# Performance work log

Measured on AMD Instinct MI355X. Metric: run time of the kernel, lower is better.

Reference implementation:

```python
import jax, jax.numpy as jnp
import numpy as np
from jax import lax

HID = 768          # hidden_dim / embedding_dim
IN = 64            # input_dim = max_seq_length // num_heads
SEQ = 512          # max_seq_length
GROUPS = IN        # conv groups
BLUR_K = 5
BLUR_SIGMA = 1.0


def _gauss1d(k, sigma):
    half = (k - 1) * 0.5
    x = np.linspace(-half, half, k)
    pdf = np.exp(-0.5 * (x / sigma) ** 2)
    return pdf / pdf.sum()


def setup_inputs() -> dict:
    key = jax.random.key(0)
    ks = jax.random.split(key, 8)
    s = 0.02
    return {
        "inputs": jax.random.normal(ks[0], (16, SEQ, HID), jnp.float32),
        # Conv1d(768, 768, k=3, groups=64): weight [out_ch, in_ch/groups, k]
        "conv_w": jax.random.normal(ks[1], (HID, HID // GROUPS, 3), jnp.float32) * s,
        "conv_b": jnp.zeros((HID,), jnp.float32),
        "ln_g": jnp.ones((IN,), jnp.float32),
        "ln_b": jnp.zeros((IN,), jnp.float32),
        # function_info: Linear(64, 64), torch weight convention [out, in]
        "fi_w": jax.random.normal(ks[2], (IN, IN), jnp.float32) * s,
        "fi_b": jnp.zeros((IN,), jnp.float32),
        # block_info: Linear(64, 1)
        "bi_w": jax.random.normal(ks[3], (1, IN), jnp.float32) * s,
        "bi_b": jnp.zeros((1,), jnp.float32),
    }


def _forward(inputs, conv_w, conv_b, ln_g, ln_b, fi_w, fi_b, bi_w, bi_b):
    x = inputs.reshape(-1, HID, IN)  # [Bn, 768, 64] (raw row-major view, as torch .view)
    q = k = v = m = x

    # q: grouped Conv1d + residual, GELU, LayerNorm over last dim (64)
    qc = lax.conv_general_dilated(
        q, conv_w, window_strides=(1,), padding=[(1, 1)],
        feature_group_count=GROUPS, dimension_numbers=("NCH", "OIH", "NCH"))
    qc = qc + conv_b[None, :, None]
    q = jax.nn.gelu(qc + q, approximate=False)
    mu = jnp.mean(q, axis=-1, keepdims=True)
    var = jnp.mean(jnp.square(q - mu), axis=-1, keepdims=True)
    q = (q - mu) * lax.rsqrt(var + 1e-5) * ln_g + ln_b

    # v: Linear(64,64) + GELU
    v = jax.nn.gelu(v @ fi_w.T + fi_b, approximate=False)

    # k: dropout (eval -> identity), softmax over dim=-2 (channel axis), GELU
    k = jax.nn.gelu(jax.nn.softmax(k, axis=-2), approximate=False)

    # m: GaussianBlur(5, sigma fixed 1.0) over (H=768, W=64) with reflect pad, then Linear(64,1)
    g = _gauss1d(BLUR_K, BLUR_SIGMA)
    kern = jnp.asarray(np.outer(g, g), m.dtype)[None, None]  # [1,1,5,5]
    p = BLUR_K // 2
    mp = jnp.pad(m[:, None], ((0, 0), (0, 0), (p, p), (p, p)), mode="reflect")
    m = lax.conv_general_dilated(
        mp, kern, (1, 1), "VALID", dimension_numbers=("NCHW", "OIHW", "NCHW"))[:, 0]
    m = m @ bi_w.T + bi_b                        # [Bn, 768, 1]
    mask = jnp.broadcast_to(m, (m.shape[0], HID, HID))  # expand to [Bn,768,768]

    # SDPA: scale = 1/sqrt(E) with E = q.shape[-1] = 64; additive float mask
    scores = jnp.einsum("bce,bde->bcd", q, k) * (1.0 / np.sqrt(IN)) + mask
    attn = jax.nn.softmax(scores, axis=-1)
    out = jnp.einsum("bcd,bde->bce", attn, v)    # [Bn, 768, 64]
    return out.reshape(-1, SEQ, HID)


def reference(inputs, conv_w, conv_b, ln_g, ln_b, fi_w, fi_b, bi_w, bi_b):
    return _forward(inputs, conv_w, conv_b, ln_g, ln_b, fi_w, fi_b, bi_w, bi_b)
```

## Files before the change

kernel.cpp:

```cpp
#include <hip/hip_runtime.h>
#include <hip/hip_bf16.h>
#include <math.h>

#define NB 128
#define NC 768
#define NE 64
#define IPG 12

#define QSCALE 0.18033688011112042f

typedef __hip_bfloat16 bf16;
typedef __bf16 bf16v8 __attribute__((ext_vector_type(8)));
typedef __bf16 bf16v4 __attribute__((ext_vector_type(4)));
typedef __bf16 bf16v2 __attribute__((ext_vector_type(2)));
typedef float f32x4 __attribute__((ext_vector_type(4)));
typedef float f32x16 __attribute__((ext_vector_type(16)));
typedef unsigned int u32;
typedef u32 u32x4 __attribute__((ext_vector_type(4)));

__device__ __forceinline__ float gelu_exact(float x) {
    float ax = fabsf(x);
    float t = __builtin_amdgcn_rcpf(fmaf(0.2316419f, ax, 1.0f));
    float poly = t * fmaf(t, fmaf(t, fmaf(t, fmaf(t, 1.330274429f,
                  -1.821255978f), 1.781477937f), -0.356563782f), 0.319381530f);
    float pdf = 0.3989422804f * __expf(-0.5f * ax * ax);
    float c = fmaf(-pdf, poly, 1.0f);
    float cdf = (x >= 0.f) ? c : 1.0f - c;
    return x * cdf;
}

#define MFMA16(a, b, c) __builtin_amdgcn_mfma_f32_16x16x32_bf16(a, b, c, 0, 0, 0)
#define MFMA32(a, b, c) __builtin_amdgcn_mfma_f32_32x32x16_bf16(a, b, c, 0, 0, 0)

__device__ __forceinline__ void gload_lds16(const void* g, void* l) {
    __builtin_amdgcn_global_load_lds(
        (const __attribute__((address_space(1))) void*)g,
        (__attribute__((address_space(3))) void*)l, 16, 0, 0);
}

__device__ __forceinline__ u32 pkbf(float a, float b) {
    bf16v2 t; t[0] = (__bf16)a; t[1] = (__bf16)b;
    return __builtin_bit_cast(u32, t);
}

__global__ __launch_bounds__(256) void k_conv(
    const float* __restrict__ x, const float* __restrict__ cw,
    const float* __restrict__ cb, const float* __restrict__ lg,
    const float* __restrict__ lb, bf16* __restrict__ qo,
    float* __restrict__ sp)
{
    int b = blockIdx.x >> 4;
    int chunk = blockIdx.x & 15;
    int w = threadIdx.x >> 6;
    int g = __builtin_amdgcn_readfirstlane(chunk * 4 + w);
    int h = threadIdx.x & 63;
    const float* xb = x + ((size_t)b * NC + g * IPG) * NE;

    float xi[IPG], xm[IPG], xp[IPG];
    #pragma unroll
    for (int i = 0; i < IPG; ++i) {
        xi[i] = xb[i * NE + h];
        float up = __shfl_up(xi[i], 1);
        float dn = __shfl_down(xi[i], 1);
        xm[i] = h ? up : 0.f;
        xp[i] = (h < 63) ? dn : 0.f;
    }

    float es = 0.f;
    #pragma unroll
    for (int i = 0; i < IPG; ++i) es += __expf(xi[i]);
    __shared__ float red[4][64];
    red[w][h] = es;
    __syncthreads();
    if (w == 0) {
        float s = red[0][h] + red[1][h] + red[2][h] + red[3][h];
        sp[(size_t)(b * 16 + chunk) * 64 + h] = s;
    }

    float gam = lg[h], bet = lb[h];
    const float* wg = cw + (size_t)g * IPG * 36;

    for (int o = 0; o < IPG; ++o) {
        const float* wo = wg + o * 36;
        float acc = cb[g * IPG + o];
        #pragma unroll
        for (int i = 0; i < IPG; ++i)
            acc = fmaf(xm[i], wo[i*3], fmaf(xi[i], wo[i*3+1], fmaf(xp[i], wo[i*3+2], acc)));
        float gl = gelu_exact(acc + xi[o]);
        float s1 = gl, s2 = gl * gl;
        #pragma unroll
        for (int off = 32; off; off >>= 1) {
            s1 += __shfl_xor(s1, off);
            s2 += __shfl_xor(s2, off);
        }
        float mu  = s1 * (1.f / 64.f);
        float var = s2 * (1.f / 64.f) - mu * mu;
        float qn = (gl - mu) * rsqrtf(var + 1e-5f) * gam + bet;
        qo[((size_t)b * NC + g * IPG + o) * NE + h] = __float2bfloat16(qn * QSCALE);
    }
}

__global__ __launch_bounds__(256) void k_vk(
    const float* __restrict__ x, const float* __restrict__ fw,
    const float* __restrict__ fb, const float* __restrict__ sp,
    bf16* __restrict__ ko, bf16* __restrict__ vTo)
{
    int chunk = blockIdx.x, b = blockIdx.y;
    int tid = threadIdx.x, w = tid >> 6, l = tid & 63;
    int lr = l & 15, lc = (l >> 4) * 8;
    int rowb = chunk * 64 + w * 16;
    const float* xb = x + (size_t)b * NC * NE;

    __shared__ float sts[64];
    if (tid < 64) {
        float s = 0.f;
        #pragma unroll
        for (int p = 0; p < 16; ++p) s += sp[(size_t)(b * 16 + p) * 64 + tid];
        sts[tid] = 1.f / s;
    }

    bf16v8 bfr[4][2];
    float fbias[4];
    #pragma unroll
    for (int nt = 0; nt < 4; ++nt) {
        #pragma unroll
        for (int kt = 0; kt < 2; ++kt) {
            const float* p = fw + (nt*16 + lr) * 64 + kt*32 + lc;
            bf16v8 t;
            #pragma unroll
            for (int j = 0; j < 8; ++j) t[j] = (__bf16)p[j];
            bfr[nt][kt] = t;
        }
        fbias[nt] = fb[nt*16 + lr];
    }
    __syncthreads();

    float isA[8], isB[8];
    #pragma unroll
    for (int j = 0; j < 8; ++j) { isA[j] = sts[lc + j]; isB[j] = sts[32 + lc + j]; }

    const float* pa = xb + (size_t)(rowb + lr) * NE;
    float xa[8], xc[8];
    #pragma unroll
    for (int j = 0; j < 8; ++j) xa[j] = pa[lc + j];
    #pragma unroll
    for (int j = 0; j < 8; ++j) xc[j] = pa[32 + lc + j];

    bf16v8 a0, a1;
    #pragma unroll
    for (int j = 0; j < 8; ++j) a0[j] = (__bf16)xa[j];
    #pragma unroll
    for (int j = 0; j < 8; ++j) a1[j] = (__bf16)xc[j];

    bf16v8 kv0, kv1;
    #pragma unroll
    for (int j = 0; j < 8; ++j) kv0[j] = (__bf16)gelu_exact(__expf(xa[j]) * isA[j]);
    #pragma unroll
    for (int j = 0; j < 8; ++j) kv1[j] = (__bf16)gelu_exact(__expf(xc[j]) * isB[j]);
    bf16* kp = ko + ((size_t)b * NC + rowb + lr) * NE + lc;
    *(bf16v8*)kp = kv0;
    *(bf16v8*)(kp + 32) = kv1;

    #pragma unroll
    for (int nt = 0; nt < 4; ++nt) {
        f32x4 acc = {fbias[nt], fbias[nt], fbias[nt], fbias[nt]};
        acc = MFMA16(a0, bfr[nt][0], acc);
        acc = MFMA16(a1, bfr[nt][1], acc);
        bf16v4 pk;
        #pragma unroll
        for (int r = 0; r < 4; ++r) pk[r] = (__bf16)gelu_exact(acc[r]);
        int c = rowb + (l >> 4) * 4;
        *(bf16v4*)&vTo[((size_t)b * NE + nt*16 + lr) * NC + c] = pk;
    }
}

__global__ __launch_bounds__(256, 3) void k_attn(const bf16* __restrict__ qb,
                                                 const bf16* __restrict__ kb,
                                                 const bf16* __restrict__ vT,
                                                 float* __restrict__ out) {
    __shared__ __align__(16) __bf16 ldsK[2][4096];
    __shared__ __align__(16) __bf16 ldsV[2][4096];

    int bid = blockIdx.x;
    int swz = (bid & 7) * 96 + (bid >> 3);
    int b = swz / 6, qt = swz - b * 6;
    int w = threadIdx.x >> 6, l = threadIdx.x & 63;
    int q0 = qt * 128 + w * 32;
    int l31 = l & 31, b5 = l >> 5;

    int krow_ = w * 8 + (l >> 3);
    int kc16_ = (l & 7) ^ (l >> 3);
    const char* kgbase = (const char*)(kb + (size_t)b * NC * NE)
                       + krow_ * 128 + kc16_ * 16;
    int ve_   = w * 16 + (l >> 2);
    int vc16_ = (l & 3) ^ ((l >> 3) & 3);
    const char* vgbase = (const char*)(vT + (size_t)b * NE * NC)
                       + ve_ * 1536 + vc16_ * 16;

    int krd[4];
    #pragma unroll
    for (int c = 0; c < 4; ++c)
        krd[c] = l31 * 64 + ((((c << 1) | b5) ^ (l & 7)) << 3);
    int vsw = (l31 >> 1) & 3;
    int vrd[2];
    #pragma unroll
    for (int ck = 0; ck < 2; ++ck)
        vrd[ck] = l31 * 32 + ((((ck << 1) | b5) ^ vsw) << 3);

    const bf16* qp = qb + ((size_t)b * NC + q0 + l31) * NE + b5 * 8;
    bf16v8 qf0 = *(const bf16v8*)qp;
    bf16v8 qf1 = *(const bf16v8*)(qp + 16);
    bf16v8 qf2 = *(const bf16v8*)(qp + 32);
    bf16v8 qf3 = *(const bf16v8*)(qp + 48);

    f32x16 o0 = {0,0,0,0,0,0,0,0,0,0,0,0,0,0,0,0};
    f32x16 o1 = {0,0,0,0,0,0,0,0,0,0,0,0,0,0,0,0};
    float rsum = 0.f;

    gload_lds16(kgbase,        &ldsK[0][w * 512]);
    gload_lds16(kgbase + 4096, &ldsK[0][2048 + w * 512]);
    gload_lds16(vgbase,        &ldsV[0][w * 512]);
    gload_lds16(vgbase + 64,   &ldsV[0][2048 + w * 512]);
    __syncthreads();

    int cur = 0;
    for (int ph = 0; ph < 12; ++ph) {
        if (ph < 11) {
            const char* kg = kgbase + (size_t)(2 * ph + 2) * 4096;
            gload_lds16(kg,        &ldsK[cur ^ 1][w * 512]);
            gload_lds16(kg + 4096, &ldsK[cur ^ 1][2048 + w * 512]);
            const char* vg = vgbase + (size_t)(2 * ph + 2) * 64;
            gload_lds16(vg,        &ldsV[cur ^ 1][w * 512]);
            gload_lds16(vg + 64,   &ldsV[cur ^ 1][2048 + w * 512]);
        }

        #pragma unroll
        for (int sub = 0; sub < 2; ++sub) {
            const __bf16* Kc = &ldsK[cur][sub * 2048];
            const __bf16* Vc = &ldsV[cur][sub * 2048];

            bf16v8 ka0 = *(const bf16v8*)&Kc[krd[0]];
            bf16v8 ka1 = *(const bf16v8*)&Kc[krd[1]];
            bf16v8 ka2 = *(const bf16v8*)&Kc[krd[2]];
            bf16v8 ka3 = *(const bf16v8*)&Kc[krd[3]];
            __builtin_amdgcn_s_setprio(1);
            f32x16 s = {0,0,0,0,0,0,0,0,0,0,0,0,0,0,0,0};
            s = MFMA32(ka0, qf0, s);
            s = MFMA32(ka1, qf1, s);
            s = MFMA32(ka2, qf2, s);
            s = MFMA32(ka3, qf3, s);
            __builtin_amdgcn_s_setprio(0);

            u32 wv[8];
            #pragma unroll
            for (int qd = 0; qd < 4; ++qd) {
                float a0 = exp2f(s[4*qd + 0]);
                float a1 = exp2f(s[4*qd + 1]);
                float a2 = exp2f(s[4*qd + 2]);
                float a3 = exp2f(s[4*qd + 3]);
                rsum += (a0 + a1) + (a2 + a3);
                wv[2*qd]     = pkbf(a0, a1);
                wv[2*qd + 1] = pkbf(a2, a3);
            }

            #pragma unroll
            for (int ck = 0; ck < 2; ++ck) {
                u32 y1 = (u32)__shfl_xor((int)(b5 ? wv[4*ck]     : wv[4*ck+2]), 32);
                u32 y2 = (u32)__shfl_xor((int)(b5 ? wv[4*ck + 1] : wv[4*ck+3]), 32);
                u32x4 fw_;
                fw_[0] = b5 ? y1 : wv[4*ck];
                fw_[1] = b5 ? y2 : wv[4*ck + 1];
                fw_[2] = b5 ? wv[4*ck + 2] : y1;
                fw_[3] = b5 ? wv[4*ck + 3] : y2;
                bf16v8 pf = __builtin_bit_cast(bf16v8, fw_);
                bf16v8 va0 = *(const bf16v8*)&Vc[vrd[ck]];
                bf16v8 va1 = *(const bf16v8*)&Vc[vrd[ck] + 1024];
                __builtin_amdgcn_s_setprio(1);
                o0 = MFMA32(va0, pf, o0);
                o1 = MFMA32(va1, pf, o1);
                __builtin_amdgcn_s_setprio(0);
            }
        }

        __syncthreads();
        cur ^= 1;
    }

    rsum += __shfl_xor(rsum, 32);
    float inv = 1.f / rsum;

    float* ob = out + ((size_t)b * NC + q0 + l31) * NE + b5 * 4;
    #pragma unroll
    for (int qd = 0; qd < 4; ++qd) {
        f32x4 v0, v1;
        #pragma unroll
        for (int r = 0; r < 4; ++r) {
            v0[r] = o0[4*qd + r] * inv;
            v1[r] = o1[4*qd + r] * inv;
        }
        *(f32x4*)&ob[qd * 8]      = v0;
        *(f32x4*)&ob[32 + qd * 8] = v1;
    }
}

extern "C" void kernel_launch(void* const* d_in, const int* in_sizes, int n_in,
                              void* d_out, int out_size, void* d_ws, size_t ws_size,
                              hipStream_t stream) {
    (void)in_sizes; (void)n_in; (void)out_size; (void)ws_size;
    const float* x      = (const float*)d_in[0];
    const float* conv_w = (const float*)d_in[1];
    const float* conv_b = (const float*)d_in[2];
    const float* ln_g   = (const float*)d_in[3];
    const float* ln_b   = (const float*)d_in[4];
    const float* fi_w   = (const float*)d_in[5];
    const float* fi_b   = (const float*)d_in[6];

    bf16* qbuf = (bf16*)d_ws;
    bf16* kbuf = qbuf + (size_t)NB * NC * NE;
    bf16* vT   = kbuf + (size_t)NB * NC * NE;
    float* stats = (float*)(vT + (size_t)NB * NC * NE);
    float* out = (float*)d_out;

    k_conv<<<dim3(NB * 16), 256, 0, stream>>>(x, conv_w, conv_b, ln_g, ln_b,
                                              qbuf, stats);
    k_vk<<<dim3(12, NB), 256, 0, stream>>>(x, fi_w, fi_b, stats, kbuf, vT);
    k_attn<<<dim3(768), 256, 0, stream>>>(qbuf, kbuf, vT, out);
}
```

Baseline: 82.80 us.

## Triple-buffer K/V LDS staging with explicit vmcnt waits in attention loop

Moves the attention kernel's K/V shared-memory staging from double to triple buffering, prefetching two tiles ahead. The full __syncthreads drain is replaced by partial s_waitcnt vmcnt waits and raw s_barrier calls. The goal is to keep more global-to-LDS loads in flight, so each phase's load latency is hidden behind more MFMA work. In exchange, LDS per block grows from 32KB to 48KB, which may reduce occupancy at launch_bounds(256,3). Correctness now depends on the vmcnt counts matching the number of outstanding loads.

```diff
diff --git a/kernel.cpp b/kernel.cpp
--- a/kernel.cpp
+++ b/kernel.cpp
@@ -178,8 +178,8 @@
                                                  const bf16* __restrict__ kb,
                                                  const bf16* __restrict__ vT,
                                                  float* __restrict__ out) {
-    __shared__ __align__(16) __bf16 ldsK[2][4096];
-    __shared__ __align__(16) __bf16 ldsV[2][4096];
+    __shared__ __align__(16) __bf16 ldsK[3][4096];
+    __shared__ __align__(16) __bf16 ldsV[3][4096];
 
     int bid = blockIdx.x;
     int swz = (bid & 7) * 96 + (bid >> 3);
@@ -217,22 +217,31 @@
     f32x16 o1 = {0,0,0,0,0,0,0,0,0,0,0,0,0,0,0,0};
     float rsum = 0.f;
 
-    gload_lds16(kgbase,        &ldsK[0][w * 512]);
-    gload_lds16(kgbase + 4096, &ldsK[0][2048 + w * 512]);
-    gload_lds16(vgbase,        &ldsV[0][w * 512]);
-    gload_lds16(vgbase + 64,   &ldsV[0][2048 + w * 512]);
-    __syncthreads();
+    #define STAGE(t, buf)                                                     \
+        do {                                                                  \
+            const char* kg_ = kgbase + (size_t)(2 * (t)) * 4096;              \
+            gload_lds16(kg_,        &ldsK[buf][w * 512]);                     \
+            gload_lds16(kg_ + 4096, &ldsK[buf][2048 + w * 512]);              \
+            const char* vg_ = vgbase + (size_t)(2 * (t)) * 64;                \
+            gload_lds16(vg_,        &ldsV[buf][w * 512]);                     \
+            gload_lds16(vg_ + 64,   &ldsV[buf][2048 + w * 512]);              \
+        } while (0)
+
+    STAGE(0, 0);
+    STAGE(1, 1);
 
     int cur = 0;
     for (int ph = 0; ph < 12; ++ph) {
-        if (ph < 11) {
-            const char* kg = kgbase + (size_t)(2 * ph + 2) * 4096;
-            gload_lds16(kg,        &ldsK[cur ^ 1][w * 512]);
-            gload_lds16(kg + 4096, &ldsK[cur ^ 1][2048 + w * 512]);
-            const char* vg = vgbase + (size_t)(2 * ph + 2) * 64;
-            gload_lds16(vg,        &ldsV[cur ^ 1][w * 512]);
-            gload_lds16(vg + 64,   &ldsV[cur ^ 1][2048 + w * 512]);
-        }
+        if (ph <= 9) {
+            int nbuf = (cur + 2 >= 3) ? cur - 1 : cur + 2;
+            STAGE(ph + 2, nbuf);
+            asm volatile("s_waitcnt vmcnt(8)" ::: "memory");
+        } else if (ph == 10) {
+            asm volatile("s_waitcnt vmcnt(4)" ::: "memory");
+        } else {
+            asm volatile("s_waitcnt vmcnt(0)" ::: "memory");
+        }
+        __builtin_amdgcn_s_barrier();
 
         #pragma unroll
         for (int sub = 0; sub < 2; ++sub) {
@@ -282,9 +291,10 @@
             }
         }
 
-        __syncthreads();
-        cur ^= 1;
-    }
+        __builtin_amdgcn_s_barrier();
+        cur = (cur >= 2) ? 0 : cur + 1;
+    }
+    #undef STAGE
 
     rsum += __shfl_xor(rsum, 32);
     float inv = 1.f / rsum;
```

After: 82.83 us. Within noise of the previous version (+0.0%).
